# Performance work log

Hardware: AMD Instinct MI355X
Metric: run time of the kernel (lower is better)

## Reference

```python
import jax, jax.numpy as jnp
import numpy as np

LAST_Q = 64      # queries used for dynamic pattern estimation (MInference default)
V_TOPK = 1024    # number of vertical (column) indices kept
S_TOPK = 2048    # number of slash (diagonal) offsets kept
FORCE_V = 30     # first columns always kept
FORCE_S = 100    # most-recent diagonals always kept


def setup_inputs() -> dict:
    key = jax.random.key(0)
    kq, kk, kv = jax.random.split(key, 3)
    B, H, S, D = 1, 8, 4096, 128
    q = jax.random.normal(kq, (B, H, S, D), dtype=jnp.float32)
    k = jax.random.normal(kk, (B, H, S, D), dtype=jnp.float32)
    v = jax.random.normal(kv, (B, H, S, D), dtype=jnp.float32)
    return {"q": q, "k": k, "v": v}


def _vertical_slash_attention(q, k, v):
    B, H, S, D = q.shape
    scale = 1.0 / np.sqrt(D).astype(np.float32)

    # ---- pattern estimation on the last LAST_Q queries ----
    qk = jnp.einsum('bhqd,bhkd->bhqk', q[:, :, -LAST_Q:], k) * scale  # [B,H,LQ,S]
    qpos = S - LAST_Q + jnp.arange(LAST_Q)                            # query positions
    causal_last = qpos[:, None] >= jnp.arange(S)[None, :]             # [LQ,S]
    qk = jnp.where(causal_last, qk, jnp.finfo(qk.dtype).min)
    qk = jax.nn.softmax(qk, axis=-1)

    # vertical (column) scores
    vertical = qk.sum(axis=2)                                         # [B,H,S]
    vertical = vertical.at[..., :FORCE_V].set(jnp.inf)
    v_idx = jax.lax.top_k(vertical, V_TOPK)[1]                        # column ids [B,H,V_TOPK]

    # slash (diagonal) scores, indexed by distance o = i - j in [0, S)
    dist = qpos[:, None] - jnp.arange(S)[None, :]                     # [LQ,S]
    dist_c = jnp.clip(dist, 0, S - 1)
    slash = jnp.zeros((B, H, S), qk.dtype).at[:, :, dist_c].add(
        jnp.where(dist >= 0, qk, 0.0))                                # [B,H,S]
    slash = slash.at[..., :FORCE_S].set(jnp.inf)
    s_off = jax.lax.top_k(slash, S_TOPK)[1]                           # diagonal offsets [B,H,S_TOPK]

    # ---- build vertical-slash sparsity mask ----
    ar = jnp.arange(S)
    v_mask = (v_idx[..., :, None] == ar).any(axis=-2)                 # [B,H,S] column allowed
    s_mask = (s_off[..., :, None] == ar).any(axis=-2)                 # [B,H,S] offset allowed

    dmat = ar[:, None] - ar[None, :]                                  # [S,S] query-key distance
    causal = dmat >= 0
    allowed = causal & (v_mask[:, :, None, :] | s_mask[:, :, jnp.clip(dmat, 0, S - 1)])

    # ---- sparse (mask-equivalent) attention ----
    scores = jnp.einsum('bhqd,bhkd->bhqk', q, k) * scale              # [B,H,S,S]
    scores = jnp.where(allowed, scores, jnp.finfo(scores.dtype).min)
    probs = jax.nn.softmax(scores, axis=-1)
    return jnp.einsum('bhqk,bhkd->bhqd', probs, v)


def reference(q, k, v):
    return _vertical_slash_attention(q, k, v)
```

## Files before the change

### kernel.cpp

```cpp
#include <hip/hip_runtime.h>
#include <hip/hip_bf16.h>
#include <math.h>

#define S_LEN 4096
#define DHEAD 128
#define NHEAD 8
#define LASTQ 64
#define V_TOPK 1024
#define S_TOPK 2048
#define FORCE_V 30
#define FORCE_S 100

#define SCALE 0.08838834764831845f
#define NEGBIG -3.0e38f

#define NJOBS 111

typedef __attribute__((ext_vector_type(8))) short short8;
typedef __attribute__((ext_vector_type(4))) float floatx4;
typedef unsigned long long u64;

__device__ __forceinline__ unsigned short f2bf(float f) {
    unsigned u = __float_as_uint(f);
    unsigned r = (u + 0x7fffu + ((u >> 16) & 1u)) >> 16;
    return (unsigned short)r;
}
__device__ __forceinline__ float bf2f(unsigned short s) {
    unsigned u = ((unsigned)s) << 16;
    return __uint_as_float(u);
}

__device__ const short jobQ[NJOBS] = {
    0,1,2,3,4, 5,5, 6,6, 7,7, 8,8, 9,9, 10,10,
    11,11,11, 12,12,12, 13,13,13, 14,14,14, 15,15,15,
    16,16,16,16, 17,17,17,17, 18,18,18,18, 19,19,19,19, 20,20,20,20, 21,21,21,21,
    22,22,22,22,22, 23,23,23,23,23, 24,24,24,24,24, 25,25,25,25,25, 26,26,26,26,26,
    27,27,27,27,27,27, 28,28,28,28,28,28, 29,29,29,29,29,29, 30,30,30,30,30,30,
    31,31,31,31,31,31};
__device__ const short jobK0[NJOBS] = {
    0,0,0,0,0, 0,6, 0,7, 0,8, 0,9, 0,10, 0,11,
    0,8,16, 0,9,18, 0,10,19, 0,10,20, 0,11,22,
    0,9,18,26, 0,9,18,27, 0,10,20,29, 0,10,20,30, 0,11,22,32, 0,11,22,33,
    0,10,19,28,37, 0,10,20,30,39, 0,10,20,30,40, 0,11,22,32,42, 0,11,22,33,44,
    0,10,20,29,38,47, 0,10,20,30,40,49, 0,10,20,30,40,50, 0,11,22,32,42,52,
    0,11,22,33,44,54};
__device__ const short jobK1[NJOBS] = {
    2,4,6,8,10, 6,12, 7,14, 8,16, 9,18, 10,20, 11,22,
    8,16,24, 9,18,26, 10,19,28, 10,20,30, 11,22,32,
    9,18,26,34, 9,18,27,36, 10,20,29,38, 10,20,30,40, 11,22,32,42, 11,22,33,44,
    10,19,28,37,46, 10,20,30,39,48, 10,20,30,40,50, 11,22,32,42,52, 11,22,33,44,54,
    10,20,29,38,47,56, 10,20,30,40,49,58, 10,20,30,40,50,60, 11,22,32,42,52,62,
    11,22,33,44,54,64};
__device__ const short pBase[32] = {0,1,2,3,4,5,7,9,11,13,15,17,20,23,26,29,
                                    32,36,40,44,48,52,56,61,66,71,76,81,87,93,99,105};
__device__ const short pCnt[32]  = {1,1,1,1,1,2,2,2,2,2,2,3,3,3,3,3,
                                    4,4,4,4,4,4,5,5,5,5,5,6,6,6,6,6};

__global__ __launch_bounds__(256) void prep_score(const float* __restrict__ q,
                                                  const float* __restrict__ k,
                                                  const float* __restrict__ v,
                                                  unsigned short* __restrict__ kbf,
                                                  unsigned short* __restrict__ vtbf,
                                                  float* __restrict__ scores) {
    __shared__ __align__(16) char smem[32768];
    int b = blockIdx.x, t = threadIdx.x;
    if (b < 512) {
        const float4* src = (const float4*)k;
        int base = b * 2048;
#pragma unroll
        for (int i = 0; i < 8; ++i) {
            int idx = base + i * 256 + t;
            float4 val = src[idx];
            ushort4 o;
            o.x = f2bf(val.x); o.y = f2bf(val.y); o.z = f2bf(val.z); o.w = f2bf(val.w);
            ((ushort4*)kbf)[idx] = o;
        }
    } else if (b < 1536) {
        int bx = b - 512;
        int h  = bx >> 7;
        int rem = bx & 127;
        int d0 = (rem >> 6) * 64;
        int k0 = (rem & 63) * 64;
        unsigned short (*T)[72] = (unsigned short (*)[72])smem;
#pragma unroll
        for (int it = 0; it < 4; ++it) {
            int idx = t + it * 256;
            int r = idx >> 4, c4 = idx & 15;
            float4 val = *(const float4*)(v + ((size_t)(h * S_LEN) + k0 + r) * DHEAD + d0 + c4 * 4);
            T[c4 * 4 + 0][r] = f2bf(val.x);
            T[c4 * 4 + 1][r] = f2bf(val.y);
            T[c4 * 4 + 2][r] = f2bf(val.z);
            T[c4 * 4 + 3][r] = f2bf(val.w);
        }
        __syncthreads();
#pragma unroll
        for (int it = 0; it < 2; ++it) {
            int idx = t + it * 256;
            int r = idx >> 3, c8 = idx & 7;
            *(uint4*)(vtbf + ((size_t)h * DHEAD + d0 + r) * S_LEN + k0 + c8 * 8) = *(uint4*)&T[r][c8 * 8];
        }
    } else {
        int bx = b - 1536;
        int h  = bx >> 6;
        int kt = bx & 63;
        int jl = t >> 2, part = t & 3;
        int j  = kt * 64 + jl;
        float4* Qs = (float4*)smem;
        const float4* qbase = (const float4*)(q + ((size_t)h * S_LEN + (S_LEN - LASTQ)) * DHEAD);
        for (int idx = t; idx < 64 * 32; idx += 256) Qs[idx] = qbase[idx];
        __syncthreads();

        float4 kr[8];
        const float4* kp = (const float4*)(k + ((size_t)h * S_LEN + j) * DHEAD) + part * 8;
#pragma unroll
        for (int c = 0; c < 8; ++c) kr[c] = kp[c];

        float* sp = scores + (size_t)h * LASTQ * S_LEN + j;
#pragma unroll 4
        for (int qi = 0; qi < LASTQ; ++qi) {
            const float4* qp4 = Qs + qi * 32 + part * 8;
            float dot = 0.f;
#pragma unroll
            for (int c = 0; c < 8; ++c) {
                float4 a = qp4[c], bb = kr[c];
                dot += a.x * bb.x + a.y * bb.y + a.z * bb.z + a.w * bb.w;
            }
            dot += __shfl_xor(dot, 1, 64);
            dot += __shfl_xor(dot, 2, 64);
            if (part == 0) {
                int qpos = S_LEN - LASTQ + qi;
                sp[(size_t)qi * S_LEN] = (j <= qpos) ? dot * SCALE : NEGBIG;
            }
        }
    }
}

__global__ __launch_bounds__(256) void row_stats(const float* __restrict__ scores,
                                                 float* __restrict__ m_out,
                                                 float* __restrict__ inv_out) {
    int row  = blockIdx.x * 4 + (threadIdx.x >> 6);
    int lane = threadIdx.x & 63;
    const float4* rp = (const float4*)(scores + (size_t)row * S_LEN);
    float mx = NEGBIG;
    for (int i = lane; i < S_LEN / 4; i += 64) {
        float4 s4 = rp[i];
        mx = fmaxf(mx, fmaxf(fmaxf(s4.x, s4.y), fmaxf(s4.z, s4.w)));
    }
#pragma unroll
    for (int d = 32; d >= 1; d >>= 1) mx = fmaxf(mx, __shfl_xor(mx, d, 64));
    float su = 0.f;
    for (int i = lane; i < S_LEN / 4; i += 64) {
        float4 s4 = rp[i];
        su += __expf(s4.x - mx) + __expf(s4.y - mx) + __expf(s4.z - mx) + __expf(s4.w - mx);
    }
#pragma unroll
    for (int d = 32; d >= 1; d >>= 1) su += __shfl_xor(su, d, 64);
    if (lane == 0) { m_out[row] = mx; inv_out[row] = 1.0f / su; }
}

__global__ __launch_bounds__(256) void vs_accum(const float* __restrict__ scores,
                                                const float* __restrict__ m_all,
                                                const float* __restrict__ inv_all,
                                                float* __restrict__ vertical,
                                                float* __restrict__ slash) {
    int h     = blockIdx.x >> 4;
    int chunk = blockIdx.x & 15;
    int t = threadIdx.x;
    __shared__ float sm[LASTQ], sv[LASTQ];
    if (t < LASTQ) { sm[t] = m_all[h * LASTQ + t]; sv[t] = inv_all[h * LASTQ + t]; }
    __syncthreads();

    int j = chunk * 256 + t;
    const float* S0 = scores + (size_t)h * LASTQ * S_LEN;
    float vacc = 0.f, sacc = 0.f;
    for (int r = 0; r < LASTQ; ++r) {
        vacc += __expf(S0[(size_t)r * S_LEN + j] - sm[r]) * sv[r];
        int idx = (S_LEN - LASTQ) + r - j;
        if (idx >= 0)
            sacc += __expf(S0[(size_t)r * S_LEN + idx] - sm[r]) * sv[r];
    }
    vertical[h * S_LEN + j] = vacc;
    slash[h * S_LEN + j]    = sacc;
}

__global__ __launch_bounds__(1024) void topk_mask(const float* __restrict__ vertical,
                                                  const float* __restrict__ slash,
                                                  unsigned* __restrict__ col_mask,
                                                  unsigned* __restrict__ diag_mask) {
    int h   = blockIdx.x >> 1;
    int sel = blockIdx.x & 1;
    const float* src = sel ? (slash + h * S_LEN) : (vertical + h * S_LEN);
    unsigned* dst    = sel ? (diag_mask + h * 128) : (col_mask + h * 128);
    int kwant  = sel ? S_TOPK : V_TOPK;
    int forced = sel ? FORCE_S : FORCE_V;
    int t = threadIdx.x;

    __shared__ unsigned keys[S_LEN];
    __shared__ int hist[256];
    __shared__ int sh_digit, sh_want;

#pragma unroll
    for (int rep = 0; rep < 4; ++rep) {
        int j = rep * 1024 + t;
        float f = (j < forced) ? __builtin_inff() : src[j];
        unsigned u = __float_as_uint(f);
        u = (u & 0x80000000u) ? ~u : (u | 0x80000000u);
        keys[j] = u;
    }
    __syncthreads();

    unsigned prefix = 0;
    int want = kwant;
    for (int shift = 24; shift >= 0; shift -= 8) {
        if (t < 256) hist[t] = 0;
        __syncthreads();
#pragma unroll
        for (int rep = 0; rep < 4; ++rep) {
            unsigned key = keys[rep * 1024 + t];
            bool match = (shift == 24) || (((key ^ prefix) >> (shift + 8)) == 0);
            if (match) atomicAdd(&hist[(key >> shift) & 255u], 1);
        }
        __syncthreads();
        if (t == 0) {
            int cum = 0, d = 255;
            for (; d >= 0; --d) {
                cum += hist[d];
                if (cum >= want) break;
            }
            sh_digit = d;
            sh_want  = want - (cum - hist[d]);
        }
        __syncthreads();
        prefix |= ((unsigned)sh_digit) << shift;
        want = sh_want;
        __syncthreads();
    }
    if (t < 128) {
        unsigned bits = 0;
        for (int b = 0; b < 32; ++b)
            if (keys[t * 32 + b] >= prefix) bits |= (1u << b);
        dst[t] = bits;
    }
}

#define KS_STRIDE 136
#define VT_STRIDE 72
#define PS_STRIDE 72
#define KP_ELEMS 9216

__global__ __launch_bounds__(256, 2) void sparse_attn_mfma(
        const float* __restrict__ q,
        const unsigned short* __restrict__ kbf,
        const unsigned short* __restrict__ vtbf,
        const unsigned* __restrict__ col_mask,
        const unsigned* __restrict__ diag_mask,
        unsigned short* __restrict__ pO, float* __restrict__ pl) {
    int b = blockIdx.x;
    int h = b & 7;
    int job = b >> 3;
    int Q  = jobQ[job];
    int k0 = jobK0[job];
    int k1 = jobK1[job];
    int i0 = Q * 128;
    int t    = threadIdx.x;
    int wave = t >> 6;
    int lane = t & 63;
    int ln16 = lane & 15;
    int quad = lane >> 4;

    __shared__ __align__(16) unsigned short KP[KP_ELEMS];
    __shared__ __align__(16) unsigned short Vt[128 * VT_STRIDE];
    __shared__ u64 allowed[128];
    __shared__ unsigned dmLDS[130];

    if (t < 130) dmLDS[t] = (t < 128) ? diag_mask[h * 128 + t] : 0u;

    short8 qf[2][4];
#pragma unroll
    for (int s = 0; s < 2; ++s) {
        int qrow = i0 + wave * 32 + s * 16 + ln16;
        const float* qp = q + ((size_t)h * S_LEN + qrow) * DHEAD;
#pragma unroll
        for (int ds = 0; ds < 4; ++ds) {
            int base = ds * 32 + quad * 8;
            float4 a = *(const float4*)(qp + base);
            float4 c = *(const float4*)(qp + base + 4);
            union { unsigned short u[8]; short8 v; } tmp;
            tmp.u[0] = f2bf(a.x * SCALE); tmp.u[1] = f2bf(a.y * SCALE);
            tmp.u[2] = f2bf(a.z * SCALE); tmp.u[3] = f2bf(a.w * SCALE);
            tmp.u[4] = f2bf(c.x * SCALE); tmp.u[5] = f2bf(c.y * SCALE);
            tmp.u[6] = f2bf(c.z * SCALE); tmp.u[7] = f2bf(c.w * SCALE);
            qf[s][ds] = tmp.v;
        }
    }

    floatx4 o4[2][8];
#pragma unroll
    for (int s = 0; s < 2; ++s)
#pragma unroll
        for (int n = 0; n < 8; ++n) o4[s][n] = (floatx4){0.f, 0.f, 0.f, 0.f};
    float lpart[2][4] = {{0.f, 0.f, 0.f, 0.f}, {0.f, 0.f, 0.f, 0.f}};

    unsigned short* psw[2];
    psw[0] = KP + (wave * 2 + 0) * 16 * PS_STRIDE;
    psw[1] = KP + (wave * 2 + 1) * 16 * PS_STRIDE;

    for (int jt = k0; jt < k1; ++jt) {
        int j0 = jt * 64;
        __syncthreads();

#pragma unroll
        for (int it = 0; it < 4; ++it) {
            int idx = t + it * 256;
            int r = idx >> 4, c8 = idx & 15;
            *(uint4*)&KP[r * KS_STRIDE + c8 * 8] =
                *(const uint4*)(kbf + ((size_t)(h * S_LEN) + j0 + r) * DHEAD + c8 * 8);
        }
#pragma unroll
        for (int it = 0; it < 4; ++it) {
            int idx = t + it * 256;
            int r = idx >> 3, c8 = idx & 7;
            *(uint4*)&Vt[r * VT_STRIDE + c8 * 8] =
                *(const uint4*)(vtbf + ((size_t)h * DHEAD + r) * S_LEN + j0 + c8 * 8);
        }
        if (t < 128) {
            int i = i0 + t;
            int off0 = i - j0;
            u64 a = 0;
            if (off0 >= 0) {
                u64 causal = (off0 >= 63) ? ~0ull : ((1ull << (off0 + 1)) - 1ull);
                u64 cwv = ((u64)col_mask[h * 128 + (j0 >> 5) + 1] << 32) |
                          (u64)col_mask[h * 128 + (j0 >> 5)];
                int sb = off0 - 63;
                u64 V;
                if (sb >= 0) {
                    int w = sb >> 5, sh = sb & 31;
                    u64 lo = ((u64)dmLDS[w + 1] << 32) | (u64)dmLDS[w];
                    u64 hi = (u64)dmLDS[w + 2];
                    V = (lo >> sh) | (sh ? (hi << (64 - sh)) : 0ull);
                } else {
                    u64 w0 = ((u64)dmLDS[1] << 32) | (u64)dmLDS[0];
                    V = w0 << (-sb);
                }
                a = (cwv | __brevll(V)) & causal;
            }
            allowed[t] = a;
        }
        __syncthreads();

        floatx4 sa[2][4];
#pragma unroll
        for (int s = 0; s < 2; ++s)
#pragma unroll
            for (int c = 0; c < 4; ++c) sa[s][c] = (floatx4){0.f, 0.f, 0.f, 0.f};
#pragma unroll
        for (int c = 0; c < 4; ++c) {
            const unsigned short* kbase = KP + (c * 16 + ln16) * KS_STRIDE + quad * 8;
#pragma unroll
            for (int ds = 0; ds < 4; ++ds) {
                short8 kf = *(const short8*)(kbase + ds * 32);
                sa[0][c] = __builtin_amdgcn_mfma_f32_16x16x32_bf16(qf[0][ds], kf, sa[0][c], 0, 0, 0);
                sa[1][c] = __builtin_amdgcn_mfma_f32_16x16x32_bf16(qf[1][ds], kf, sa[1][c], 0, 0, 0);
            }
        }
        __syncthreads();

#pragma unroll
        for (int s = 0; s < 2; ++s) {
            u64 Arow[4];
#pragma unroll
            for (int r = 0; r < 4; ++r)
                Arow[r] = allowed[wave * 32 + s * 16 + quad * 4 + r];
#pragma unroll
            for (int r = 0; r < 4; ++r) {
                float psum = 0.f;
#pragma unroll
                for (int c = 0; c < 4; ++c) {
                    bool ok = (Arow[r] >> (c * 16 + ln16)) & 1ull;
                    float p = ok ? __expf(sa[s][c][r]) : 0.f;
                    psw[s][(quad * 4 + r) * PS_STRIDE + c * 16 + ln16] = f2bf(p);
                    psum += p;
                }
                lpart[s][r] += psum;
            }
        }
        asm volatile("" ::: "memory");

        short8 pf[2][2];
#pragma unroll
        for (int s = 0; s < 2; ++s) {
            pf[s][0] = *(const short8*)&psw[s][ln16 * PS_STRIDE + quad * 8];
            pf[s][1] = *(const short8*)&psw[s][ln16 * PS_STRIDE + 32 + quad * 8];
        }

#pragma unroll
        for (int n = 0; n < 8; ++n) {
            const unsigned short* vbase = Vt + (n * 16 + ln16) * VT_STRIDE + quad * 8;
            short8 vf0 = *(const short8*)(vbase);
            short8 vf1 = *(const short8*)(vbase + 32);
            o4[0][n] = __builtin_amdgcn_mfma_f32_16x16x32_bf16(pf[0][0], vf0, o4[0][n], 0, 0, 0);
            o4[0][n] = __builtin_amdgcn_mfma_f32_16x16x32_bf16(pf[0][1], vf1, o4[0][n], 0, 0, 0);
            o4[1][n] = __builtin_amdgcn_mfma_f32_16x16x32_bf16(pf[1][0], vf0, o4[1][n], 0, 0, 0);
            o4[1][n] = __builtin_amdgcn_mfma_f32_16x16x32_bf16(pf[1][1], vf1, o4[1][n], 0, 0, 0);
        }
    }

    int pidx = h * NJOBS + job;
    unsigned short* pOp = pO + (size_t)pidx * (128 * DHEAD);
#pragma unroll
    for (int s = 0; s < 2; ++s)
#pragma unroll
        for (int r = 0; r < 4; ++r) {
            float su = lpart[s][r];
#pragma unroll
            for (int d = 8; d >= 1; d >>= 1) su += __shfl_xor(su, d, 64);
            int row = wave * 32 + s * 16 + quad * 4 + r;
            if (ln16 == 0) pl[pidx * 128 + row] = su;
#pragma unroll
            for (int n = 0; n < 8; ++n)
                pOp[row * DHEAD + n * 16 + ln16] = f2bf(o4[s][n][r]);
        }
}

__global__ __launch_bounds__(256) void merge_out(const unsigned short* __restrict__ pO,
                                                 const float* __restrict__ pl,
                                                 float* __restrict__ out) {
    int b = blockIdx.x;
    int h = b >> 5, Q = b & 31;
    int t = threadIdx.x;
    int row = t >> 1, half = t & 1;
    int p0 = h * NJOBS + pBase[Q];
    int cnt = pCnt[Q];

    float denom = 0.f;
    for (int p = 0; p < cnt; ++p) denom += pl[(p0 + p) * 128 + row];
    float invl = 1.0f / denom;

    float acc[64];
#pragma unroll
    for (int i = 0; i < 64; ++i) acc[i] = 0.f;
    for (int p = 0; p < cnt; ++p) {
        const unsigned short* Op = pO + (size_t)(p0 + p) * (128 * DHEAD) + row * DHEAD + half * 64;
#pragma unroll
        for (int g = 0; g < 8; ++g) {
            ushort4 u0 = ((const ushort4*)Op)[g * 2];
            ushort4 u1 = ((const ushort4*)Op)[g * 2 + 1];
            acc[g * 8 + 0] += bf2f(u0.x); acc[g * 8 + 1] += bf2f(u0.y);
            acc[g * 8 + 2] += bf2f(u0.z); acc[g * 8 + 3] += bf2f(u0.w);
            acc[g * 8 + 4] += bf2f(u1.x); acc[g * 8 + 5] += bf2f(u1.y);
            acc[g * 8 + 6] += bf2f(u1.z); acc[g * 8 + 7] += bf2f(u1.w);
        }
    }
    float* op = out + ((size_t)h * S_LEN + Q * 128 + row) * DHEAD + half * 64;
#pragma unroll
    for (int g = 0; g < 16; ++g) {
        float4 c;
        c.x = acc[g * 4 + 0] * invl; c.y = acc[g * 4 + 1] * invl;
        c.z = acc[g * 4 + 2] * invl; c.w = acc[g * 4 + 3] * invl;
        ((float4*)op)[g] = c;
    }
}

extern "C" void kernel_launch(void* const* d_in, const int* in_sizes, int n_in,
                              void* d_out, int out_size, void* d_ws, size_t ws_size,
                              hipStream_t stream) {
    const float* q = (const float*)d_in[0];
    const float* k = (const float*)d_in[1];
    const float* v = (const float*)d_in[2];
    float* out = (float*)d_out;

    unsigned* col_m  = (unsigned*)d_ws;
    unsigned* diag_m = col_m + 1024;
    float* m_all    = (float*)(diag_m + 1024);
    float* inv_all  = m_all + 512;
    float* vertical = inv_all + 512;
    float* slash    = vertical + NHEAD * S_LEN;
    unsigned short* kbf  = (unsigned short*)(slash + NHEAD * S_LEN);
    unsigned short* vtbf = kbf + (size_t)NHEAD * S_LEN * DHEAD;
    float* scores = (float*)(vtbf + (size_t)NHEAD * S_LEN * DHEAD);
    unsigned short* pO = (unsigned short*)(scores + (size_t)NHEAD * LASTQ * S_LEN);
    float* pl = (float*)(pO + (size_t)8 * NJOBS * 128 * DHEAD);

    prep_score<<<2048, 256, 0, stream>>>(q, k, v, kbf, vtbf, scores);
    row_stats<<<NHEAD * LASTQ / 4, 256, 0, stream>>>(scores, m_all, inv_all);
    vs_accum<<<NHEAD * 16, 256, 0, stream>>>(scores, m_all, inv_all, vertical, slash);
    topk_mask<<<NHEAD * 2, 1024, 0, stream>>>(vertical, slash, col_m, diag_m);
    sparse_attn_mfma<<<NHEAD * NJOBS, 256, 0, stream>>>(q, kbf, vtbf, col_m, diag_m, pO, pl);
    merge_out<<<NHEAD * 32, 256, 0, stream>>>(pO, pl, out);
}
```

Baseline: 303.6 us.

## Fuse softmax row sums into scoring, parallelize top-k scan, prefetch K/V tiles

Removes the row_stats kernel by computing per-tile exp sums in prep_score, skipping max subtraction. vs_accum then sums those partials to get the softmax normalizers. The top-k radix digit search now uses a 64-lane shuffle suffix scan instead of a serial single-thread loop. The sparse attention kernel prefetches the next K/V tile into registers while the current tile is being computed. Dropping the max subtraction risks exp overflow for large scores, and the prefetch raises register pressure.

```diff
diff --git a/kernel.cpp b/kernel.cpp
--- a/kernel.cpp
+++ b/kernel.cpp
@@ -61,8 +61,9 @@
                                                   const float* __restrict__ v,
                                                   unsigned short* __restrict__ kbf,
                                                   unsigned short* __restrict__ vtbf,
-                                                  float* __restrict__ scores) {
-    __shared__ __align__(16) char smem[32768];
+                                                  float* __restrict__ scores,
+                                                  float* __restrict__ Zpart) {
+    __shared__ __align__(16) char smem[33792];
     int b = blockIdx.x, t = threadIdx.x;
     if (b < 512) {
         const float4* src = (const float4*)k;
@@ -104,8 +105,10 @@
         int h  = bx >> 6;
         int kt = bx & 63;
         int jl = t >> 2, part = t & 3;
+        int lane = t & 63, wave = t >> 6;
         int j  = kt * 64 + jl;
         float4* Qs = (float4*)smem;
+        float* Zw  = (float*)(smem + 32768);
         const float4* qbase = (const float4*)(q + ((size_t)h * S_LEN + (S_LEN - LASTQ)) * DHEAD);
         for (int idx = t; idx < 64 * 32; idx += 256) Qs[idx] = qbase[idx];
         __syncthreads();
@@ -127,57 +130,56 @@
             }
             dot += __shfl_xor(dot, 1, 64);
             dot += __shfl_xor(dot, 2, 64);
+            int qpos = S_LEN - LASTQ + qi;
+            bool vis = (j <= qpos);
+            float e = 0.f;
             if (part == 0) {
-                int qpos = S_LEN - LASTQ + qi;
-                sp[(size_t)qi * S_LEN] = (j <= qpos) ? dot * SCALE : NEGBIG;
-            }
-        }
-    }
-}
-
-__global__ __launch_bounds__(256) void row_stats(const float* __restrict__ scores,
-                                                 float* __restrict__ m_out,
-                                                 float* __restrict__ inv_out) {
-    int row  = blockIdx.x * 4 + (threadIdx.x >> 6);
-    int lane = threadIdx.x & 63;
-    const float4* rp = (const float4*)(scores + (size_t)row * S_LEN);
-    float mx = NEGBIG;
-    for (int i = lane; i < S_LEN / 4; i += 64) {
-        float4 s4 = rp[i];
-        mx = fmaxf(mx, fmaxf(fmaxf(s4.x, s4.y), fmaxf(s4.z, s4.w)));
-    }
-#pragma unroll
-    for (int d = 32; d >= 1; d >>= 1) mx = fmaxf(mx, __shfl_xor(mx, d, 64));
-    float su = 0.f;
-    for (int i = lane; i < S_LEN / 4; i += 64) {
-        float4 s4 = rp[i];
-        su += __expf(s4.x - mx) + __expf(s4.y - mx) + __expf(s4.z - mx) + __expf(s4.w - mx);
-    }
-#pragma unroll
-    for (int d = 32; d >= 1; d >>= 1) su += __shfl_xor(su, d, 64);
-    if (lane == 0) { m_out[row] = mx; inv_out[row] = 1.0f / su; }
+                float s = dot * SCALE;
+                sp[(size_t)qi * S_LEN] = vis ? s : NEGBIG;
+                e = vis ? __expf(s) : 0.f;
+            }
+            e += __shfl_xor(e, 4, 64);
+            e += __shfl_xor(e, 8, 64);
+            e += __shfl_xor(e, 16, 64);
+            e += __shfl_xor(e, 32, 64);
+            if (lane == 0) Zw[wave * 64 + qi] = e;
+        }
+        __syncthreads();
+        if (t < 64) {
+            float z = Zw[0 * 64 + t] + Zw[1 * 64 + t] + Zw[2 * 64 + t] + Zw[3 * 64 + t];
+            Zpart[((size_t)(h * LASTQ + t)) * 64 + kt] = z;
+        }
+    }
 }
 
 __global__ __launch_bounds__(256) void vs_accum(const float* __restrict__ scores,
-                                                const float* __restrict__ m_all,
-                                                const float* __restrict__ inv_all,
+                                                const float* __restrict__ Zpart,
                                                 float* __restrict__ vertical,
                                                 float* __restrict__ slash) {
     int h     = blockIdx.x >> 4;
     int chunk = blockIdx.x & 15;
     int t = threadIdx.x;
-    __shared__ float sm[LASTQ], sv[LASTQ];
-    if (t < LASTQ) { sm[t] = m_all[h * LASTQ + t]; sv[t] = inv_all[h * LASTQ + t]; }
+    __shared__ float sv[LASTQ];
+    if (t < LASTQ) {
+        const float4* zp = (const float4*)(Zpart + (size_t)(h * LASTQ + t) * 64);
+        float z = 0.f;
+#pragma unroll
+        for (int i = 0; i < 16; ++i) {
+            float4 a = zp[i];
+            z += a.x + a.y + a.z + a.w;
+        }
+        sv[t] = 1.0f / z;
+    }
     __syncthreads();
 
     int j = chunk * 256 + t;
     const float* S0 = scores + (size_t)h * LASTQ * S_LEN;
     float vacc = 0.f, sacc = 0.f;
     for (int r = 0; r < LASTQ; ++r) {
-        vacc += __expf(S0[(size_t)r * S_LEN + j] - sm[r]) * sv[r];
+        vacc += __expf(S0[(size_t)r * S_LEN + j]) * sv[r];
         int idx = (S_LEN - LASTQ) + r - j;
         if (idx >= 0)
-            sacc += __expf(S0[(size_t)r * S_LEN + idx] - sm[r]) * sv[r];
+            sacc += __expf(S0[(size_t)r * S_LEN + idx]) * sv[r];
     }
     vertical[h * S_LEN + j] = vacc;
     slash[h * S_LEN + j]    = sacc;
@@ -221,14 +223,26 @@
             if (match) atomicAdd(&hist[(key >> shift) & 255u], 1);
         }
         __syncthreads();
-        if (t == 0) {
-            int cum = 0, d = 255;
-            for (; d >= 0; --d) {
-                cum += hist[d];
-                if (cum >= want) break;
-            }
-            sh_digit = d;
-            sh_want  = want - (cum - hist[d]);
+        if (t < 64) {
+            int b0 = hist[4 * t], b1 = hist[4 * t + 1], b2 = hist[4 * t + 2], b3 = hist[4 * t + 3];
+            int s3 = b3, s2 = b2 + s3, s1 = b1 + s2, s0 = b0 + s1;
+            int suf = s0;
+#pragma unroll
+            for (int d = 1; d < 64; d <<= 1) {
+                int o = __shfl_down(suf, d, 64);
+                if (t + d < 64) suf += o;
+            }
+            int above = suf - s0;
+            int sufs0 = s0 + above, sufs1 = s1 + above, sufs2 = s2 + above, sufs3 = s3 + above;
+            int sv_[4] = {sufs0, sufs1, sufs2, sufs3};
+#pragma unroll
+            for (int i = 0; i < 4; ++i) {
+                int nxt = (i < 3) ? sv_[i + 1] : above;
+                if (sv_[i] >= want && nxt < want) {
+                    sh_digit = 4 * t + i;
+                    sh_want  = want - nxt;
+                }
+            }
         }
         __syncthreads();
         prefix |= ((unsigned)sh_digit) << shift;
@@ -305,23 +319,38 @@
     psw[0] = KP + (wave * 2 + 0) * 16 * PS_STRIDE;
     psw[1] = KP + (wave * 2 + 1) * 16 * PS_STRIDE;
 
-    for (int jt = k0; jt < k1; ++jt) {
-        int j0 = jt * 64;
-        __syncthreads();
-
+    uint4 kr[4], vr[4];
+    {
+        int j0 = k0 * 64;
 #pragma unroll
         for (int it = 0; it < 4; ++it) {
             int idx = t + it * 256;
             int r = idx >> 4, c8 = idx & 15;
-            *(uint4*)&KP[r * KS_STRIDE + c8 * 8] =
-                *(const uint4*)(kbf + ((size_t)(h * S_LEN) + j0 + r) * DHEAD + c8 * 8);
+            kr[it] = *(const uint4*)(kbf + ((size_t)(h * S_LEN) + j0 + r) * DHEAD + c8 * 8);
         }
 #pragma unroll
         for (int it = 0; it < 4; ++it) {
             int idx = t + it * 256;
             int r = idx >> 3, c8 = idx & 7;
-            *(uint4*)&Vt[r * VT_STRIDE + c8 * 8] =
-                *(const uint4*)(vtbf + ((size_t)h * DHEAD + r) * S_LEN + j0 + c8 * 8);
+            vr[it] = *(const uint4*)(vtbf + ((size_t)h * DHEAD + r) * S_LEN + j0 + c8 * 8);
+        }
+    }
+
+    for (int jt = k0; jt < k1; ++jt) {
+        int j0 = jt * 64;
+        __syncthreads();
+
+#pragma unroll
+        for (int it = 0; it < 4; ++it) {
+            int idx = t + it * 256;
+            int r = idx >> 4, c8 = idx & 15;
+            *(uint4*)&KP[r * KS_STRIDE + c8 * 8] = kr[it];
+        }
+#pragma unroll
+        for (int it = 0; it < 4; ++it) {
+            int idx = t + it * 256;
+            int r = idx >> 3, c8 = idx & 7;
+            *(uint4*)&Vt[r * VT_STRIDE + c8 * 8] = vr[it];
         }
         if (t < 128) {
             int i = i0 + t;
@@ -348,6 +377,22 @@
         }
         __syncthreads();
 
+        if (jt + 1 < k1) {
+            int jn = j0 + 64;
+#pragma unroll
+            for (int it = 0; it < 4; ++it) {
+                int idx = t + it * 256;
+                int r = idx >> 4, c8 = idx & 15;
+                kr[it] = *(const uint4*)(kbf + ((size_t)(h * S_LEN) + jn + r) * DHEAD + c8 * 8);
+            }
+#pragma unroll
+            for (int it = 0; it < 4; ++it) {
+                int idx = t + it * 256;
+                int r = idx >> 3, c8 = idx & 7;
+                vr[it] = *(const uint4*)(vtbf + ((size_t)h * DHEAD + r) * S_LEN + jn + c8 * 8);
+            }
+        }
+
         floatx4 sa[2][4];
 #pragma unroll
         for (int s = 0; s < 2; ++s)
@@ -471,9 +516,8 @@
 
     unsigned* col_m  = (unsigned*)d_ws;
     unsigned* diag_m = col_m + 1024;
-    float* m_all    = (float*)(diag_m + 1024);
-    float* inv_all  = m_all + 512;
-    float* vertical = inv_all + 512;
+    float* Zpart    = (float*)(diag_m + 1024);
+    float* vertical = Zpart + NHEAD * LASTQ * 64;
     float* slash    = vertical + NHEAD * S_LEN;
     unsigned short* kbf  = (unsigned short*)(slash + NHEAD * S_LEN);
     unsigned short* vtbf = kbf + (size_t)NHEAD * S_LEN * DHEAD;
@@ -481,9 +525,8 @@
     unsigned short* pO = (unsigned short*)(scores + (size_t)NHEAD * LASTQ * S_LEN);
     float* pl = (float*)(pO + (size_t)8 * NJOBS * 128 * DHEAD);
 
-    prep_score<<<2048, 256, 0, stream>>>(q, k, v, kbf, vtbf, scores);
-    row_stats<<<NHEAD * LASTQ / 4, 256, 0, stream>>>(scores, m_all, inv_all);
-    vs_accum<<<NHEAD * 16, 256, 0, stream>>>(scores, m_all, inv_all, vertical, slash);
+    prep_score<<<2048, 256, 0, stream>>>(q, k, v, kbf, vtbf, scores, Zpart);
+    vs_accum<<<NHEAD * 16, 256, 0, stream>>>(scores, Zpart, vertical, slash);
     topk_mask<<<NHEAD * 2, 1024, 0, stream>>>(vertical, slash, col_m, diag_m);
     sparse_attn_mfma<<<NHEAD * NJOBS, 256, 0, stream>>>(q, kbf, vtbf, col_m, diag_m, pO, pl);
     merge_out<<<NHEAD * 32, 256, 0, stream>>>(pO, pl, out);
```

Result: slower. 320.3 us (+5.5%).
